# Performance work log

Hardware: AMD Instinct MI355X
Metric: run time of the kernel (lower is better)

The kernel has to match this reference:

```python
import jax, jax.numpy as jnp
import numpy as np

TEMPERATURE = 0.1
EPS = 1e-8


def setup_inputs() -> dict:
    key = jax.random.key(0)
    k1, k2 = jax.random.split(key)
    N, D = 4096, 256
    z_i = jax.random.normal(k1, (N, D), dtype=jnp.float32)
    z_j = jax.random.normal(k2, (N, D), dtype=jnp.float32)
    return {"z_i": z_i, "z_j": z_j}


def reference(z_i, z_j):
    N = z_i.shape[0]
    zi = z_i.reshape(N, -1)
    zj = z_j.reshape(N, -1)
    z = jnp.concatenate([zi, zj], axis=0)  # [2N, D]
    # cosine similarity: normalize rows once, then a single GEMM
    norms = jnp.linalg.norm(z, axis=1, keepdims=True)
    zn = z / jnp.maximum(norms, EPS)
    sim = zn @ zn.T  # [2N, 2N]
    idx = jnp.arange(N)
    sim_ij = sim[idx, idx + N]   # diag offset +N
    sim_ji = sim[idx + N, idx]   # diag offset -N
    positives = jnp.concatenate([sim_ij, sim_ji], axis=0)  # [2N]
    # denominator: row-mean of exp(sim / t) over all 2N columns (incl. self)
    denom_mean = jnp.mean(jnp.exp(sim / TEMPERATURE), axis=1)  # [2N]
    all_losses = -(positives / TEMPERATURE - jnp.log(denom_mean))
    loss = jnp.sum(all_losses) / (2 * N)
    return loss
```

## Files before the change

kernel.cpp:

```cpp
#include <hip/hip_runtime.h>
#include <hip/hip_bf16.h>
#include <math.h>

#define NN 4096
#define DD 256
#define TWO_N 8192
#define SCALE 14.426950408889634f
#define INV_2N (1.0f/8192.0f)

typedef __bf16 bf16_t;
typedef bf16_t bf16x8 __attribute__((ext_vector_type(8)));
typedef bf16_t bf16x4 __attribute__((ext_vector_type(4)));
typedef float f32x4 __attribute__((ext_vector_type(4)));

__global__ __launch_bounds__(256) void knorm(const float* __restrict__ zi,
                                             const float* __restrict__ zj,
                                             bf16_t* __restrict__ zn,
                                             float* __restrict__ rowsum,
                                             float* __restrict__ possum,
                                             float* __restrict__ out) {
    const int wid = threadIdx.x >> 6, lane = threadIdx.x & 63;
    const int b = blockIdx.x;
    if (b < 8) {
        f32x4 z = {0, 0, 0, 0};
        *(f32x4*)(rowsum + b * 1024 + threadIdx.x * 4) = z;
        if (b == 0 && threadIdx.x == 0) { possum[0] = 0.0f; out[0] = 0.0f; }
    }
    const int row = b * 4 + wid;
    const float* src = (row < NN) ? (zi + (size_t)row * DD)
                                  : (zj + (size_t)(row - NN) * DD);
    float4 v = *(const float4*)(src + lane * 4);
    float ss = v.x*v.x + v.y*v.y + v.z*v.z + v.w*v.w;
    #pragma unroll
    for (int m = 1; m < 64; m <<= 1) ss += __shfl_xor(ss, m);
    const float sc = 1.0f / fmaxf(sqrtf(ss), 1e-8f);
    bf16x4 o;
    o[0] = (bf16_t)(v.x * sc);
    o[1] = (bf16_t)(v.y * sc);
    o[2] = (bf16_t)(v.z * sc);
    o[3] = (bf16_t)(v.w * sc);
    *(bf16x4*)(zn + (size_t)row * DD + lane * 4) = o;
}

__global__ __launch_bounds__(256, 4) void kmain(const bf16_t* __restrict__ zn,
                                                float* __restrict__ rowsum,
                                                float* __restrict__ possum) {
    __shared__ char ldsA[16384];
    __shared__ char ldsB[16384];
    const int tid = threadIdx.x, wid = tid >> 6, lane = tid & 63;

    int ti = 0, rem = blockIdx.x;
    while (rem >= 64 - ti) { rem -= 64 - ti; ++ti; }
    const int tj = ti + rem;
    const int rowbase = ti << 7, colbase = tj << 7;

    const int wr = wid >> 1, wc = wid & 1;
    const int lo = lane & 15, hi = lane >> 4;

    f32x4 acc[4][4];
    #pragma unroll
    for (int s = 0; s < 4; ++s)
        #pragma unroll
        for (int t = 0; t < 4; ++t) acc[s][t] = (f32x4){0, 0, 0, 0};

    const char* gz = (const char*)zn;

    for (int ks = 0; ks < 4; ++ks) {
        #pragma unroll
        for (int p = 0; p < 4; ++p) {
            const int base = p * 4096 + wid * 1024;
            const int dd   = base + lane * 16;
            const int row  = dd >> 7, col = dd & 127;
            const int scol = col ^ ((row & 7) << 4);
            const char* ga = gz + (size_t)(rowbase + row) * 512 + ks * 128 + scol;
            const char* gb = gz + (size_t)(colbase + row) * 512 + ks * 128 + scol;
            __builtin_amdgcn_global_load_lds(
                (const __attribute__((address_space(1))) void*)ga,
                (__attribute__((address_space(3))) void*)(&ldsA[base]), 16, 0, 0);
            __builtin_amdgcn_global_load_lds(
                (const __attribute__((address_space(1))) void*)gb,
                (__attribute__((address_space(3))) void*)(&ldsB[base]), 16, 0, 0);
        }
        __syncthreads();

        #pragma unroll
        for (int kk = 0; kk < 2; ++kk) {
            bf16x8 af[4], bfr[4];
            const int kb = kk * 64 + hi * 16;
            const int sw = kb ^ ((lo & 7) << 4);
            #pragma unroll
            for (int s = 0; s < 4; ++s) {
                af[s]  = *(const bf16x8*)(&ldsA[(wr * 64 + s * 16 + lo) * 128 + sw]);
                bfr[s] = *(const bf16x8*)(&ldsB[(wc * 64 + s * 16 + lo) * 128 + sw]);
            }
            #pragma unroll
            for (int s = 0; s < 4; ++s)
                #pragma unroll
                for (int t = 0; t < 4; ++t)
                    acc[s][t] = __builtin_amdgcn_mfma_f32_16x16x32_bf16(
                        af[s], bfr[t], acc[s][t], 0, 0, 0);
        }
        __syncthreads();
    }

    if (tj == ti + 32 && wr == wc) {
        const int j = lo - hi * 4;
        float p = 0.0f;
        if (j >= 0 && j < 4) {
            #pragma unroll
            for (int s = 0; s < 4; ++s) p += acc[s][s][j];
        }
        #pragma unroll
        for (int m = 1; m < 64; m <<= 1) p += __shfl_xor(p, m);
        if (lane == 0) atomicAdd(possum, p);
    }

    #pragma unroll
    for (int s = 0; s < 4; ++s)
        #pragma unroll
        for (int t = 0; t < 4; ++t)
            #pragma unroll
            for (int j = 0; j < 4; ++j)
                acc[s][t][j] = __builtin_amdgcn_exp2f(acc[s][t][j] * SCALE);

    #pragma unroll
    for (int s = 0; s < 4; ++s) {
        f32x4 rs = acc[s][0] + acc[s][1] + acc[s][2] + acc[s][3];
        #pragma unroll
        for (int j = 0; j < 4; ++j) {
            float v = rs[j];
            v += __shfl_xor(v, 1); v += __shfl_xor(v, 2);
            v += __shfl_xor(v, 4); v += __shfl_xor(v, 8);
            if (lo == 0)
                atomicAdd(&rowsum[rowbase + wr * 64 + s * 16 + hi * 4 + j], v);
        }
    }

    if (ti != tj) {
        #pragma unroll
        for (int t = 0; t < 4; ++t) {
            float v = 0.0f;
            #pragma unroll
            for (int s = 0; s < 4; ++s)
                v += acc[s][t][0] + acc[s][t][1] + acc[s][t][2] + acc[s][t][3];
            v += __shfl_xor(v, 16); v += __shfl_xor(v, 32);
            if (hi == 0)
                atomicAdd(&rowsum[colbase + wc * 64 + t * 16 + lo], v);
        }
    }
}

__global__ __launch_bounds__(256) void kfinal(const float* __restrict__ rowsum,
                                              const float* __restrict__ possum,
                                              float* __restrict__ out) {
    __shared__ float red[4];
    const int wid = threadIdx.x >> 6, lane = threadIdx.x & 63;
    const int gid = blockIdx.x * 256 + threadIdx.x;
    float v = logf(rowsum[gid] * INV_2N);
    #pragma unroll
    for (int m = 1; m < 64; m <<= 1) v += __shfl_xor(v, m);
    if (lane == 0) red[wid] = v;
    __syncthreads();
    if (threadIdx.x == 0) {
        float s = red[0] + red[1] + red[2] + red[3];
        if (blockIdx.x == 0) s -= 20.0f * possum[0];
        atomicAdd(out, s * INV_2N);
    }
}

extern "C" void kernel_launch(void* const* d_in, const int* in_sizes, int n_in,
                              void* d_out, int out_size, void* d_ws, size_t ws_size,
                              hipStream_t stream) {
    const float* zi = (const float*)d_in[0];
    const float* zj = (const float*)d_in[1];
    bf16_t* zn     = (bf16_t*)d_ws;
    float*  rowsum = (float*)((char*)d_ws + (size_t)TWO_N * DD * 2);
    float*  possum = rowsum + TWO_N;
    float*  out    = (float*)d_out;

    knorm <<<2048, 256, 0, stream>>>(zi, zj, zn, rowsum, possum, out);
    kmain <<<2080, 256, 0, stream>>>(zn, rowsum, possum);
    kfinal<<<32,   256, 0, stream>>>(rowsum, possum, out);
}
```

Measured before the change: 103.1 us.

## Replace atomic row-sum accumulation with per-tile partial buffers and XCD-aware tile order

Each GEMM tile now writes its row and column exp-sums into dedicated slots in two partial-sum buffers (PR, PC) instead of issuing global atomicAdds onto a shared rowsum array. The final kernel then reduces those partials per row deterministically, which removes the need to zero rowsum in the norm kernel. Block IDs are remapped so neighbouring tiles land on the same XCD, aiming at better L2 reuse of the normalized rows. The diagonal self-similarity on diagonal tiles is forced to exactly 1.0. The tradeoff is a larger, serial reduction in kfinal (up to 128 loads per thread) and a few MB of extra workspace traffic.

```diff
diff --git a/kernel.cpp b/kernel.cpp
--- a/kernel.cpp
+++ b/kernel.cpp
@@ -16,16 +16,11 @@
 __global__ __launch_bounds__(256) void knorm(const float* __restrict__ zi,
                                              const float* __restrict__ zj,
                                              bf16_t* __restrict__ zn,
-                                             float* __restrict__ rowsum,
                                              float* __restrict__ possum,
                                              float* __restrict__ out) {
     const int wid = threadIdx.x >> 6, lane = threadIdx.x & 63;
     const int b = blockIdx.x;
-    if (b < 8) {
-        f32x4 z = {0, 0, 0, 0};
-        *(f32x4*)(rowsum + b * 1024 + threadIdx.x * 4) = z;
-        if (b == 0 && threadIdx.x == 0) { possum[0] = 0.0f; out[0] = 0.0f; }
-    }
+    if (b == 0 && threadIdx.x == 0) { possum[0] = 0.0f; out[0] = 0.0f; }
     const int row = b * 4 + wid;
     const float* src = (row < NN) ? (zi + (size_t)row * DD)
                                   : (zj + (size_t)(row - NN) * DD);
@@ -43,13 +38,17 @@
 }
 
 __global__ __launch_bounds__(256, 4) void kmain(const bf16_t* __restrict__ zn,
-                                                float* __restrict__ rowsum,
+                                                float* __restrict__ PR,
+                                                float* __restrict__ PC,
                                                 float* __restrict__ possum) {
     __shared__ char ldsA[16384];
     __shared__ char ldsB[16384];
     const int tid = threadIdx.x, wid = tid >> 6, lane = tid & 63;
 
-    int ti = 0, rem = blockIdx.x;
+    const int bid = (int)blockIdx.x;
+    const int wg  = (bid & 7) * 260 + (bid >> 3);
+
+    int ti = 0, rem = wg;
     while (rem >= 64 - ti) { rem -= 64 - ti; ++ti; }
     const int tj = ti + rem;
     const int rowbase = ti << 7, colbase = tj << 7;
@@ -115,6 +114,14 @@
         if (lane == 0) atomicAdd(possum, p);
     }
 
+    if (ti == tj && wr == wc) {
+        const int j = lo - hi * 4;
+        if (j >= 0 && j < 4) {
+            #pragma unroll
+            for (int s = 0; s < 4; ++s) acc[s][s][j] = 1.0f;
+        }
+    }
+
     #pragma unroll
     for (int s = 0; s < 4; ++s)
         #pragma unroll
@@ -123,20 +130,23 @@
             for (int j = 0; j < 4; ++j)
                 acc[s][t][j] = __builtin_amdgcn_exp2f(acc[s][t][j] * SCALE);
 
-    #pragma unroll
-    for (int s = 0; s < 4; ++s) {
-        f32x4 rs = acc[s][0] + acc[s][1] + acc[s][2] + acc[s][3];
-        #pragma unroll
-        for (int j = 0; j < 4; ++j) {
-            float v = rs[j];
-            v += __shfl_xor(v, 1); v += __shfl_xor(v, 2);
-            v += __shfl_xor(v, 4); v += __shfl_xor(v, 8);
-            if (lo == 0)
-                atomicAdd(&rowsum[rowbase + wr * 64 + s * 16 + hi * 4 + j], v);
+    {
+        float* PRb = PR + (((size_t)(ti * 64 + tj) * 2 + wc) << 7) + wr * 64;
+        #pragma unroll
+        for (int s = 0; s < 4; ++s) {
+            f32x4 rs = acc[s][0] + acc[s][1] + acc[s][2] + acc[s][3];
+            #pragma unroll
+            for (int j = 0; j < 4; ++j) {
+                float v = rs[j];
+                v += __shfl_xor(v, 1); v += __shfl_xor(v, 2);
+                v += __shfl_xor(v, 4); v += __shfl_xor(v, 8);
+                if (lo == 0) PRb[s * 16 + hi * 4 + j] = v;
+            }
         }
     }
 
     if (ti != tj) {
+        float* PCb = PC + (((size_t)(tj * 64 + ti) * 2 + wr) << 7) + wc * 64;
         #pragma unroll
         for (int t = 0; t < 4; ++t) {
             float v = 0.0f;
@@ -144,26 +154,36 @@
             for (int s = 0; s < 4; ++s)
                 v += acc[s][t][0] + acc[s][t][1] + acc[s][t][2] + acc[s][t][3];
             v += __shfl_xor(v, 16); v += __shfl_xor(v, 32);
-            if (hi == 0)
-                atomicAdd(&rowsum[colbase + wc * 64 + t * 16 + lo], v);
-        }
-    }
-}
-
-__global__ __launch_bounds__(256) void kfinal(const float* __restrict__ rowsum,
+            if (hi == 0) PCb[t * 16 + lo] = v;
+        }
+    }
+}
+
+__global__ __launch_bounds__(128) void kfinal(const float* __restrict__ PR,
+                                              const float* __restrict__ PC,
                                               const float* __restrict__ possum,
                                               float* __restrict__ out) {
-    __shared__ float red[4];
+    __shared__ float red[2];
+    const int a = blockIdx.x;
+    const int rr = threadIdx.x;
     const int wid = threadIdx.x >> 6, lane = threadIdx.x & 63;
-    const int gid = blockIdx.x * 256 + threadIdx.x;
-    float v = logf(rowsum[gid] * INV_2N);
+    float total = 0.0f;
+    for (int t = a; t < 64; ++t) {
+        total += PR[(((size_t)(a * 64 + t) * 2 + 0) << 7) + rr];
+        total += PR[(((size_t)(a * 64 + t) * 2 + 1) << 7) + rr];
+    }
+    for (int b = 0; b < a; ++b) {
+        total += PC[(((size_t)(a * 64 + b) * 2 + 0) << 7) + rr];
+        total += PC[(((size_t)(a * 64 + b) * 2 + 1) << 7) + rr];
+    }
+    float v = logf(total * INV_2N);
     #pragma unroll
     for (int m = 1; m < 64; m <<= 1) v += __shfl_xor(v, m);
     if (lane == 0) red[wid] = v;
     __syncthreads();
     if (threadIdx.x == 0) {
-        float s = red[0] + red[1] + red[2] + red[3];
-        if (blockIdx.x == 0) s -= 20.0f * possum[0];
+        float s = red[0] + red[1];
+        if (a == 0) s -= 20.0f * possum[0];
         atomicAdd(out, s * INV_2N);
     }
 }
@@ -174,11 +194,12 @@
     const float* zi = (const float*)d_in[0];
     const float* zj = (const float*)d_in[1];
     bf16_t* zn     = (bf16_t*)d_ws;
-    float*  rowsum = (float*)((char*)d_ws + (size_t)TWO_N * DD * 2);
-    float*  possum = rowsum + TWO_N;
+    float*  PR     = (float*)((char*)d_ws + ((size_t)4 << 20));
+    float*  PC     = (float*)((char*)d_ws + ((size_t)8 << 20));
+    float*  possum = (float*)((char*)d_ws + ((size_t)12 << 20));
     float*  out    = (float*)d_out;
 
-    knorm <<<2048, 256, 0, stream>>>(zi, zj, zn, rowsum, possum, out);
-    kmain <<<2080, 256, 0, stream>>>(zn, rowsum, possum);
-    kfinal<<<32,   256, 0, stream>>>(rowsum, possum, out);
-}
+    knorm <<<2048, 256, 0, stream>>>(zi, zj, zn, possum, out);
+    kmain <<<2080, 256, 0, stream>>>(zn, PR, PC, possum);
+    kfinal<<<64,   128, 0, stream>>>(PR, PC, possum, out);
+}
```

New measurement: 106.2 us. +3.0%, slower.
